# Kernel tuning notes

Measured on AMD Instinct MI355X. Metric: run time of the kernel, lower is better.

Reference implementation:

```python
import jax, jax.numpy as jnp
import numpy as np

DIM = 64  # number of flow dimensions (block count)


def _masks(out_f, in_f, dim):
    # mask_d: 1 on the dim diagonal blocks; mask_o: 1 strictly below-block (lower-triangular off-diagonal)
    opd, ipd = out_f // dim, in_f // dim
    mask_d = np.zeros((out_f, in_f), np.float32)
    mask_o = np.ones((out_f, in_f), np.float32)
    for i in range(dim):
        mask_d[i * opd:(i + 1) * opd, i * ipd:(i + 1) * ipd] = 1.0
        mask_o[i * opd:(i + 1) * opd, i * ipd:] = 0.0
    return jnp.asarray(mask_d), jnp.asarray(mask_o)


def setup_inputs() -> dict:
    key = jax.random.key(0)
    k1, k2, k3, k4, k5 = jax.random.split(key, 5)
    B, F = 1024, 2048
    inputs = jax.random.normal(k1, (B, F), jnp.float32)
    # log-diagonal Jacobian blocks from a previous layer with per-dim input size 1
    grad = jax.random.normal(k2, (B, DIM, F // DIM, 1), jnp.float32)
    weight = jax.random.normal(k3, (F, F), jnp.float32) * 0.05
    diag_weight = jnp.log(jax.random.uniform(k4, (F, 1), jnp.float32, 1e-3, 1.0))
    bias = jax.random.uniform(k5, (F,), jnp.float32, -1.0, 1.0) / jnp.sqrt(jnp.float32(F))
    return {"inputs": inputs, "grad": grad, "weight": weight,
            "diag_weight": diag_weight, "bias": bias}


def reference(inputs, grad, weight, diag_weight, bias):
    out_f, in_f = weight.shape
    dim = DIM
    opd, ipd = out_f // dim, in_f // dim
    mask_d, mask_o = _masks(out_f, in_f, dim)

    # weight normalization with positive diagonal blocks
    w = jnp.exp(weight) * mask_d + weight * mask_o              # (out, in)
    wsn = jnp.sum(w * w, axis=-1, keepdims=True)                # (out, 1)
    w_n = jnp.exp(diag_weight) * w / jnp.sqrt(wsn)              # (out, in)
    wpl = diag_weight + weight - 0.5 * jnp.log(wsn)             # (out, in)

    out = inputs @ w_n.T + bias                                 # (B, out)

    # diagonal blocks of wpl, already transposed per-block: (dim, opd, ipd)
    wpl4 = wpl.reshape(dim, opd, dim, ipd)
    blocks = wpl4[jnp.arange(dim), :, jnp.arange(dim), :]

    B = inputs.shape[0]
    g = jnp.broadcast_to(blocks[None], (B, dim, opd, ipd))

    # combine with previous log-Jacobian: logsumexp over contracted axis
    grad_t = jnp.swapaxes(grad, -1, -2)                         # (B, dim, p, ipd)
    logdet = jax.nn.logsumexp(g[:, :, :, None, :] + grad_t[:, :, None, :, :], axis=-1)  # (B, dim, opd, p)
    return (out, logdet)
```

## Files before the change

### kernel.cpp

```cpp
#include <hip/hip_runtime.h>

#define F 2048
#define BATCH 1024

typedef short bf16x8 __attribute__((ext_vector_type(8)));
typedef float f32x4 __attribute__((ext_vector_type(4)));
typedef unsigned short u16x4 __attribute__((ext_vector_type(4)));

__device__ __forceinline__ unsigned short f2bf(float f) {
  unsigned u = __builtin_bit_cast(unsigned, f);
  unsigned r = (u + 0x7fffu + ((u >> 16) & 1u)) >> 16;
  return (unsigned short)r;
}

__device__ __forceinline__ void gload_lds16(const void* g, void* l) {
  __builtin_amdgcn_global_load_lds(
      (const __attribute__((address_space(1))) unsigned int*)g,
      (__attribute__((address_space(3))) unsigned int*)l,
      16, 0, 0);
}

__global__ __launch_bounds__(256) void prep_convert_kernel(
    const float* __restrict__ inputs, unsigned short* __restrict__ a_bf,
    const float* __restrict__ weight, const float* __restrict__ dw,
    unsigned short* __restrict__ w_n, float* __restrict__ exp_blocks)
{
  int bid = blockIdx.x;
  if (bid < 1024) {
    int idx = bid * 2048 + threadIdx.x * 8;
    float4 v0 = *(const float4*)(inputs + idx);
    float4 v1 = *(const float4*)(inputs + idx + 4);
    union { unsigned short s[8]; bf16x8 v; } o;
    o.s[0] = f2bf(v0.x); o.s[1] = f2bf(v0.y); o.s[2] = f2bf(v0.z); o.s[3] = f2bf(v0.w);
    o.s[4] = f2bf(v1.x); o.s[5] = f2bf(v1.y); o.s[6] = f2bf(v1.z); o.s[7] = f2bf(v1.w);
    *(bf16x8*)(a_bf + idx) = o.v;
    return;
  }
  int rb = bid - 1024;
  int lane = threadIdx.x & 63;
  int r = rb * 4 + (threadIdx.x >> 6);
  int i = r >> 5;
  int lim = (i + 1) * 32;
  int wlim = (r & ~63) + 64;
  int d0 = i * 32;
  const float* wrow = weight + (size_t)r * F;

  float ss = 0.f;
  for (int j = lane; j < lim / 4; j += 64) {
    float4 v = ((const float4*)wrow)[j];
    if (j * 4 >= d0) {
      v.x = __expf(v.x); v.y = __expf(v.y); v.z = __expf(v.z); v.w = __expf(v.w);
    }
    ss += v.x * v.x + v.y * v.y + v.z * v.z + v.w * v.w;
  }
#pragma unroll
  for (int d = 32; d > 0; d >>= 1) ss += __shfl_xor(ss, d, 64);

  float dwr = dw[r];
  float scale = __expf(dwr) * rsqrtf(ss);
  float halflog = 0.5f * __logf(ss);

  unsigned short* onrow = w_n + (size_t)r * F;
  for (int j = lane; j < wlim / 4; j += 64) {
    u16x4 o = {0, 0, 0, 0};
    if (j * 4 < lim) {
      float4 v = ((const float4*)wrow)[j];
      if (j * 4 >= d0) {
        v.x = __expf(v.x); v.y = __expf(v.y); v.z = __expf(v.z); v.w = __expf(v.w);
      }
      o[0] = f2bf(scale * v.x); o[1] = f2bf(scale * v.y);
      o[2] = f2bf(scale * v.z); o[3] = f2bf(scale * v.w);
    }
    *(u16x4*)(onrow + j * 4) = o;
  }
  if (lane < 32) {
    exp_blocks[(size_t)r * 32 + lane] = __expf(dwr + wrow[d0 + lane] - halflog);
  }
}

__global__ __launch_bounds__(256) void gemm_logdet_kernel(
    const unsigned short* __restrict__ A, const unsigned short* __restrict__ W,
    const float* __restrict__ bias, const float* __restrict__ grad,
    const float* __restrict__ exp_blocks, float* __restrict__ out,
    float* __restrict__ ld)
{
  __shared__ __align__(16) char smem[4 * 16384];

  int id = blockIdx.x;
  int tid = threadIdx.x;
  int lane = tid & 63, wid = tid >> 6;
  int l15 = lane & 15, lg = lane >> 4;

  if (id < 256) {
    int tm = id >> 4;
    int p  = id & 15;
    int m0 = tm * 64;
    int n0a = p * 64;
    int n0b = (31 - p) * 64;
    int nk1 = p + 1;

    int wm = wid >> 1, wn = wid & 1;
    int srow = lane >> 3;
    int schunk = (lane & 7) ^ (srow & 7);

    auto stage = [&](int s) {
      int n0, kt;
      if (s < nk1) { n0 = n0a; kt = s; } else { n0 = n0b; kt = s - nk1; }
      size_t kb = (size_t)kt * 128;
      char* base = smem + (s & 3) * 16384;
#pragma unroll
      for (int e = 0; e < 2; ++e) {
        int sg = wid * 2 + e;
        int row = sg * 8 + srow;
        gload_lds16((const char*)A + (size_t)(m0 + row) * 4096 + kb + schunk * 16,
                    base + sg * 1024);
        gload_lds16((const char*)W + (size_t)(n0 + row) * 4096 + kb + schunk * 16,
                    base + 8192 + sg * 1024);
      }
    };

    f32x4 acc_a[2][2] = {};
    f32x4 acc_b[2][2] = {};

    auto compute = [&](int s, f32x4 (*acc)[2]) {
      const char* sA = smem + (s & 3) * 16384;
      const char* sB = sA + 8192;
      bf16x8 af[2][2], bfr[2][2];
#pragma unroll
      for (int mi = 0; mi < 2; ++mi) {
        int row = wm * 32 + mi * 16 + l15;
#pragma unroll
        for (int ks = 0; ks < 2; ++ks) {
          int ch = (ks * 4 + lg) ^ (row & 7);
          af[mi][ks] = *(const bf16x8*)(sA + row * 128 + ch * 16);
        }
      }
#pragma unroll
      for (int ni = 0; ni < 2; ++ni) {
        int row = wn * 32 + ni * 16 + l15;
#pragma unroll
        for (int ks = 0; ks < 2; ++ks) {
          int ch = (ks * 4 + lg) ^ (row & 7);
          bfr[ni][ks] = *(const bf16x8*)(sB + row * 128 + ch * 16);
        }
      }
#pragma unroll
      for (int ks = 0; ks < 2; ++ks)
#pragma unroll
        for (int mi = 0; mi < 2; ++mi)
#pragma unroll
          for (int ni = 0; ni < 2; ++ni)
            acc[mi][ni] = __builtin_amdgcn_mfma_f32_16x16x32_bf16(
                af[mi][ks], bfr[ni][ks], acc[mi][ni], 0, 0, 0);
    };

    stage(0); stage(1); stage(2);
    int s = 0;
    for (; s < nk1; ++s) {
      if (s + 3 < 33) stage(s + 3);
      int rem = 32 - s;
      if (rem >= 3)      asm volatile("s_waitcnt vmcnt(12)" ::: "memory");
      else if (rem == 2) asm volatile("s_waitcnt vmcnt(8)" ::: "memory");
      else if (rem == 1) asm volatile("s_waitcnt vmcnt(4)" ::: "memory");
      else               asm volatile("s_waitcnt vmcnt(0)" ::: "memory");
      __builtin_amdgcn_s_barrier();
      compute(s, acc_a);
      __builtin_amdgcn_s_barrier();
    }
    for (; s < 33; ++s) {
      if (s + 3 < 33) stage(s + 3);
      int rem = 32 - s;
      if (rem >= 3)      asm volatile("s_waitcnt vmcnt(12)" ::: "memory");
      else if (rem == 2) asm volatile("s_waitcnt vmcnt(8)" ::: "memory");
      else if (rem == 1) asm volatile("s_waitcnt vmcnt(4)" ::: "memory");
      else               asm volatile("s_waitcnt vmcnt(0)" ::: "memory");
      __builtin_amdgcn_s_barrier();
      compute(s, acc_b);
      __builtin_amdgcn_s_barrier();
    }

#pragma unroll
    for (int t = 0; t < 2; ++t) {
      int n0 = t ? n0b : n0a;
      f32x4 (*acc)[2] = t ? acc_b : acc_a;
      float bv0 = bias[n0 + wn * 32 + l15];
      float bv1 = bias[n0 + wn * 32 + 16 + l15];
#pragma unroll
      for (int mi = 0; mi < 2; ++mi)
#pragma unroll
        for (int ni = 0; ni < 2; ++ni) {
          float bv = ni ? bv1 : bv0;
#pragma unroll
          for (int j = 0; j < 4; ++j) {
            int m = m0 + wm * 32 + mi * 16 + lg * 4 + j;
            int n = n0 + wn * 32 + ni * 16 + l15;
            out[(size_t)m * F + n] = acc[mi][ni][j] + bv;
          }
        }
    }
  } else {
    int lid = id - 256;
    int i = lid & 63;
    int bq = lid >> 6;
    int b_base = bq * 256 + wid * 64;

    const float* ebp = exp_blocks + (size_t)i * 1024;
    bf16x8 eb_lo, eb_hi;
    {
      float4 a0 = *(const float4*)(ebp + l15 * 32 + lg * 8);
      float4 a1 = *(const float4*)(ebp + l15 * 32 + lg * 8 + 4);
      float4 b0 = *(const float4*)(ebp + (16 + l15) * 32 + lg * 8);
      float4 b1 = *(const float4*)(ebp + (16 + l15) * 32 + lg * 8 + 4);
      union { unsigned short s[8]; bf16x8 v; } plo, phi;
      plo.s[0] = f2bf(a0.x); plo.s[1] = f2bf(a0.y); plo.s[2] = f2bf(a0.z); plo.s[3] = f2bf(a0.w);
      plo.s[4] = f2bf(a1.x); plo.s[5] = f2bf(a1.y); plo.s[6] = f2bf(a1.z); plo.s[7] = f2bf(a1.w);
      phi.s[0] = f2bf(b0.x); phi.s[1] = f2bf(b0.y); phi.s[2] = f2bf(b0.z); phi.s[3] = f2bf(b0.w);
      phi.s[4] = f2bf(b1.x); phi.s[5] = f2bf(b1.y); phi.s[6] = f2bf(b1.z); phi.s[7] = f2bf(b1.w);
      eb_lo = plo.v; eb_hi = phi.v;
    }

    const f32x4 zero = {0.f, 0.f, 0.f, 0.f};
#pragma unroll
    for (int g = 0; g < 4; ++g) {
      int brow = b_base + g * 16 + l15;
      const float* gp = grad + (size_t)brow * 2048 + i * 32 + lg * 8;
      float4 g0 = *(const float4*)gp;
      float4 g1 = *(const float4*)(gp + 4);
      union { unsigned short s[8]; bf16x8 v; } pg;
      pg.s[0] = f2bf(__expf(g0.x)); pg.s[1] = f2bf(__expf(g0.y));
      pg.s[2] = f2bf(__expf(g0.z)); pg.s[3] = f2bf(__expf(g0.w));
      pg.s[4] = f2bf(__expf(g1.x)); pg.s[5] = f2bf(__expf(g1.y));
      pg.s[6] = f2bf(__expf(g1.z)); pg.s[7] = f2bf(__expf(g1.w));

      f32x4 dlo = __builtin_amdgcn_mfma_f32_16x16x32_bf16(pg.v, eb_lo, zero, 0, 0, 0);
      f32x4 dhi = __builtin_amdgcn_mfma_f32_16x16x32_bf16(pg.v, eb_hi, zero, 0, 0, 0);

#pragma unroll
      for (int j = 0; j < 4; ++j) {
        int bb = b_base + g * 16 + lg * 4 + j;
        float* dst = ld + ((size_t)bb * 64 + i) * 32;
        dst[l15] = __logf(dlo[j]);
        dst[16 + l15] = __logf(dhi[j]);
      }
    }
  }
}

extern "C" void kernel_launch(void* const* d_in, const int* in_sizes, int n_in,
                              void* d_out, int out_size, void* d_ws, size_t ws_size,
                              hipStream_t stream)
{
  const float* inputs = (const float*)d_in[0];
  const float* grad   = (const float*)d_in[1];
  const float* weight = (const float*)d_in[2];
  const float* dw     = (const float*)d_in[3];
  const float* bias   = (const float*)d_in[4];

  float* out = (float*)d_out;
  float* ld  = out + (size_t)BATCH * F;

  unsigned short* w_n  = (unsigned short*)d_ws;
  unsigned short* a_bf = w_n + (size_t)F * F;
  float* exp_blocks    = (float*)(a_bf + (size_t)BATCH * F);

  prep_convert_kernel<<<1536, 256, 0, stream>>>(inputs, a_bf, weight, dw, w_n, exp_blocks);
  gemm_logdet_kernel<<<512, 256, 0, stream>>>(a_bf, w_n, bias, grad, exp_blocks, out, ld);
}
```

Before: 99.87 us.

## Split paired triangular GEMM tiles into one tile per block, largest first

```diff
diff --git a/kernel.cpp b/kernel.cpp
--- a/kernel.cpp
+++ b/kernel.cpp
@@ -78,36 +78,32 @@
   }
 }
 
-__global__ __launch_bounds__(256) void gemm_logdet_kernel(
+__global__ __launch_bounds__(256, 3) void gemm_logdet_kernel(
     const unsigned short* __restrict__ A, const unsigned short* __restrict__ W,
     const float* __restrict__ bias, const float* __restrict__ grad,
     const float* __restrict__ exp_blocks, float* __restrict__ out,
     float* __restrict__ ld)
 {
-  __shared__ __align__(16) char smem[4 * 16384];
+  __shared__ __align__(16) char smem[3 * 16384];
 
   int id = blockIdx.x;
   int tid = threadIdx.x;
   int lane = tid & 63, wid = tid >> 6;
   int l15 = lane & 15, lg = lane >> 4;
 
-  if (id < 256) {
-    int tm = id >> 4;
-    int p  = id & 15;
-    int m0 = tm * 64;
-    int n0a = p * 64;
-    int n0b = (31 - p) * 64;
-    int nk1 = p + 1;
+  if (id < 512) {
+    int tn = 31 - (id >> 4);
+    int tm = id & 15;
+    int m0 = tm * 64, n0 = tn * 64;
+    int nkt = tn + 1;
 
     int wm = wid >> 1, wn = wid & 1;
     int srow = lane >> 3;
     int schunk = (lane & 7) ^ (srow & 7);
 
-    auto stage = [&](int s) {
-      int n0, kt;
-      if (s < nk1) { n0 = n0a; kt = s; } else { n0 = n0b; kt = s - nk1; }
+    auto stage = [&](int kt) {
       size_t kb = (size_t)kt * 128;
-      char* base = smem + (s & 3) * 16384;
+      char* base = smem + (kt % 3) * 16384;
 #pragma unroll
       for (int e = 0; e < 2; ++e) {
         int sg = wid * 2 + e;
@@ -119,11 +115,10 @@
       }
     };
 
-    f32x4 acc_a[2][2] = {};
-    f32x4 acc_b[2][2] = {};
-
-    auto compute = [&](int s, f32x4 (*acc)[2]) {
-      const char* sA = smem + (s & 3) * 16384;
+    f32x4 acc[2][2] = {};
+
+    auto compute = [&](int kt) {
+      const char* sA = smem + (kt % 3) * 16384;
       const char* sB = sA + 8192;
       bf16x8 af[2][2], bfr[2][2];
 #pragma unroll
@@ -154,52 +149,35 @@
                 af[mi][ks], bfr[ni][ks], acc[mi][ni], 0, 0, 0);
     };
 
-    stage(0); stage(1); stage(2);
-    int s = 0;
-    for (; s < nk1; ++s) {
-      if (s + 3 < 33) stage(s + 3);
-      int rem = 32 - s;
-      if (rem >= 3)      asm volatile("s_waitcnt vmcnt(12)" ::: "memory");
-      else if (rem == 2) asm volatile("s_waitcnt vmcnt(8)" ::: "memory");
+    stage(0);
+    if (nkt > 1) stage(1);
+    for (int kt = 0; kt < nkt; ++kt) {
+      if (kt + 2 < nkt) stage(kt + 2);
+      int rem = nkt - 1 - kt;
+      if (rem >= 2)      asm volatile("s_waitcnt vmcnt(8)" ::: "memory");
       else if (rem == 1) asm volatile("s_waitcnt vmcnt(4)" ::: "memory");
       else               asm volatile("s_waitcnt vmcnt(0)" ::: "memory");
       __builtin_amdgcn_s_barrier();
-      compute(s, acc_a);
+      compute(kt);
       __builtin_amdgcn_s_barrier();
     }
-    for (; s < 33; ++s) {
-      if (s + 3 < 33) stage(s + 3);
-      int rem = 32 - s;
-      if (rem >= 3)      asm volatile("s_waitcnt vmcnt(12)" ::: "memory");
-      else if (rem == 2) asm volatile("s_waitcnt vmcnt(8)" ::: "memory");
-      else if (rem == 1) asm volatile("s_waitcnt vmcnt(4)" ::: "memory");
-      else               asm volatile("s_waitcnt vmcnt(0)" ::: "memory");
-      __builtin_amdgcn_s_barrier();
-      compute(s, acc_b);
-      __builtin_amdgcn_s_barrier();
-    }
-
-#pragma unroll
-    for (int t = 0; t < 2; ++t) {
-      int n0 = t ? n0b : n0a;
-      f32x4 (*acc)[2] = t ? acc_b : acc_a;
-      float bv0 = bias[n0 + wn * 32 + l15];
-      float bv1 = bias[n0 + wn * 32 + 16 + l15];
-#pragma unroll
-      for (int mi = 0; mi < 2; ++mi)
-#pragma unroll
-        for (int ni = 0; ni < 2; ++ni) {
-          float bv = ni ? bv1 : bv0;
-#pragma unroll
-          for (int j = 0; j < 4; ++j) {
-            int m = m0 + wm * 32 + mi * 16 + lg * 4 + j;
-            int n = n0 + wn * 32 + ni * 16 + l15;
-            out[(size_t)m * F + n] = acc[mi][ni][j] + bv;
-          }
+
+    float bv0 = bias[n0 + wn * 32 + l15];
+    float bv1 = bias[n0 + wn * 32 + 16 + l15];
+#pragma unroll
+    for (int mi = 0; mi < 2; ++mi)
+#pragma unroll
+      for (int ni = 0; ni < 2; ++ni) {
+        float bv = ni ? bv1 : bv0;
+#pragma unroll
+        for (int j = 0; j < 4; ++j) {
+          int m = m0 + wm * 32 + mi * 16 + lg * 4 + j;
+          int n = n0 + wn * 32 + ni * 16 + l15;
+          out[(size_t)m * F + n] = acc[mi][ni][j] + bv;
         }
-    }
+      }
   } else {
-    int lid = id - 256;
+    int lid = id - 512;
     int i = lid & 63;
     int bq = lid >> 6;
     int b_base = bq * 256 + wid * 64;
@@ -264,5 +242,5 @@
   float* exp_blocks    = (float*)(a_bf + (size_t)BATCH * F);
 
   prep_convert_kernel<<<1536, 256, 0, stream>>>(inputs, a_bf, weight, dw, w_n, exp_blocks);
-  gemm_logdet_kernel<<<512, 256, 0, stream>>>(a_bf, w_n, bias, grad, exp_blocks, out, ld);
-}
+  gemm_logdet_kernel<<<768, 256, 0, stream>>>(a_bf, w_n, bias, grad, exp_blocks, out, ld);
+}
```

Result: no change. 99.46 us (-0.4%).
